# Performance work log

Measured on AMD Instinct MI355X. Metric: run time of the kernel, lower is better.

Reference implementation:

```python
import jax, jax.numpy as jnp
import numpy as np

B, T, C, H = 2, 2048, 1024, 16
D = C // H  # head dim = 64


def setup_inputs() -> dict:
    key = jax.random.key(0)
    ks = jax.random.split(key, 5)
    s = 0.02
    return {
        "x": jax.random.normal(ks[0], (B, T, C), dtype=jnp.float32),
        "c_attn_w": jax.random.normal(ks[1], (C, 3 * C), dtype=jnp.float32) * s,
        "c_attn_b": jax.random.normal(ks[2], (3 * C,), dtype=jnp.float32) * s,
        "c_proj_w": jax.random.normal(ks[3], (C, C), dtype=jnp.float32) * s,
        "c_proj_b": jax.random.normal(ks[4], (C,), dtype=jnp.float32) * s,
    }


def reference(x, c_attn_w, c_attn_b, c_proj_w, c_proj_b):
    b, t, c = x.shape
    # GPT-2 Conv1D: x @ W + b
    qkv = x @ c_attn_w + c_attn_b                      # [B,T,3C]
    q, k, v = jnp.split(qkv, 3, axis=-1)
    # [B,H,T,D]
    q = q.reshape(b, t, H, D).transpose(0, 2, 1, 3)
    k = k.reshape(b, t, H, D).transpose(0, 2, 1, 3)
    v = v.reshape(b, t, H, D).transpose(0, 2, 1, 3)
    scale = 1.0 / jnp.sqrt(jnp.float32(D))
    scores = jnp.einsum("bhqd,bhkd->bhqk", q, k) * scale  # [B,H,T,T]
    causal = jnp.tril(jnp.ones((t, t), dtype=bool))
    scores = jnp.where(causal, scores, jnp.float32(-jnp.inf))
    attn = jax.nn.softmax(scores, axis=-1)
    # drop_rate = 0.0 -> dropout is identity
    y = jnp.einsum("bhqk,bhkd->bhqd", attn, v)          # [B,H,T,D]
    y = y.transpose(0, 2, 1, 3).reshape(b, t, c)
    return y @ c_proj_w + c_proj_b
```

## Files before the change

kernel.cpp:

```cpp
#include <hip/hip_runtime.h>

#define B_ 2
#define T_ 2048
#define C_ 1024
#define H_ 16
#define D_ 64
#define M_ (B_ * T_)
#define NQKV_ (3 * C_)

typedef unsigned short us16;
typedef short bf16x8 __attribute__((ext_vector_type(8)));
typedef float f32x4 __attribute__((ext_vector_type(4)));

__device__ __forceinline__ f32x4 mfma16(bf16x8 a, bf16x8 b, f32x4 c) {
    return __builtin_amdgcn_mfma_f32_16x16x32_bf16(a, b, c, 0, 0, 0);
}

__device__ __forceinline__ us16 f2bf(float f) {
    union { float f; unsigned int u; } v; v.f = f;
    unsigned int r = v.u + 0x7fffu + ((v.u >> 16) & 1u);
    return (us16)(r >> 16);
}

__device__ __forceinline__ void gl_lds16(const us16* g, us16* l) {
    __builtin_amdgcn_global_load_lds(
        (const __attribute__((address_space(1))) void*)g,
        (__attribute__((address_space(3))) void*)l,
        16, 0, 0);
}

__global__ __launch_bounds__(256) void cvt_bf16(
    const float* __restrict__ in, us16* __restrict__ out, int n8)
{
    const int i = blockIdx.x * blockDim.x + threadIdx.x;
    if (i >= n8) return;
    const float4 a = ((const float4*)in)[2 * i];
    const float4 b = ((const float4*)in)[2 * i + 1];
    ushort4 lo = { f2bf(a.x), f2bf(a.y), f2bf(a.z), f2bf(a.w) };
    ushort4 hi = { f2bf(b.x), f2bf(b.y), f2bf(b.z), f2bf(b.w) };
    ((ushort4*)out)[2 * i] = lo;
    ((ushort4*)out)[2 * i + 1] = hi;
}

__global__ __launch_bounds__(256) void transpose_cvt(
    const float* __restrict__ W, us16* __restrict__ Wt, int K, int N)
{
    __shared__ float tile[32][33];
    const int n0 = blockIdx.x * 32, k0 = blockIdx.y * 32;
    const int t = threadIdx.x;
    {
        const int k = t >> 3, n4 = (t & 7) * 4;
        const float4 v = *(const float4*)(W + (size_t)(k0 + k) * N + n0 + n4);
        tile[k][n4 + 0] = v.x; tile[k][n4 + 1] = v.y;
        tile[k][n4 + 2] = v.z; tile[k][n4 + 3] = v.w;
    }
    __syncthreads();
    {
        const int n = t >> 3, k4 = (t & 7) * 4;
        ushort4 o = { f2bf(tile[k4 + 0][n]), f2bf(tile[k4 + 1][n]),
                      f2bf(tile[k4 + 2][n]), f2bf(tile[k4 + 3][n]) };
        *(ushort4*)(Wt + (size_t)(n0 + n) * K + k0 + k4) = o;
    }
}

__global__ __launch_bounds__(256) void gemm_bf16(
    const us16* __restrict__ A, const us16* __restrict__ Bt,
    const float* __restrict__ bias, void* __restrict__ Cout,
    int M, int N, int K, int out_bf16)
{
    __shared__ __align__(16) us16 smem[128 * 136];
    us16* sA = smem;
    us16* sB = smem + 128 * 64;

    const int tid = threadIdx.x;
    const int lane = tid & 63, wave = tid >> 6;
    const int wr = wave >> 1, wc = wave & 1;
    const int cq = lane & 15, quad = lane >> 4;
    const int m0 = blockIdx.y * 128, n0 = blockIdx.x * 128;

    const int srow  = lane >> 3;
    const int sgran = (lane & 7) ^ srow;
    const int scol  = sgran * 8;

    f32x4 acc[4][4];
    #pragma unroll
    for (int i = 0; i < 4; ++i)
        #pragma unroll
        for (int j = 0; j < 4; ++j)
            acc[i][j] = (f32x4){0.f, 0.f, 0.f, 0.f};

    for (int k0 = 0; k0 < K; k0 += 64) {
        #pragma unroll
        for (int p = 0; p < 4; ++p) {
            const int r = p * 32 + wave * 8;
            gl_lds16(A  + (size_t)(m0 + r + srow) * K + k0 + scol, sA + r * 64);
            gl_lds16(Bt + (size_t)(n0 + r + srow) * K + k0 + scol, sB + r * 64);
        }
        __syncthreads();

        #pragma unroll
        for (int kk = 0; kk < 64; kk += 32) {
            const int koS = (((kk >> 3) + quad) ^ (cq & 7)) << 3;
            bf16x8 af[4], bfg[4];
            #pragma unroll
            for (int i = 0; i < 4; ++i) {
                af[i]  = *(const bf16x8*)(sA + (wr * 64 + i * 16 + cq) * 64 + koS);
                bfg[i] = *(const bf16x8*)(sB + (wc * 64 + i * 16 + cq) * 64 + koS);
            }
            #pragma unroll
            for (int mi = 0; mi < 4; ++mi)
                #pragma unroll
                for (int ni = 0; ni < 4; ++ni)
                    acc[mi][ni] = mfma16(af[mi], bfg[ni], acc[mi][ni]);
        }
        __syncthreads();
    }

    if (out_bf16) {
        us16* Cs = smem;
        #pragma unroll
        for (int mi = 0; mi < 4; ++mi)
            #pragma unroll
            for (int ni = 0; ni < 4; ++ni) {
                const int n = n0 + wc * 64 + ni * 16 + cq;
                const float bv = bias[n];
                #pragma unroll
                for (int r = 0; r < 4; ++r)
                    Cs[(wr * 64 + mi * 16 + quad * 4 + r) * 136 +
                       wc * 64 + ni * 16 + cq] = f2bf(acc[mi][ni][r] + bv);
            }
        __syncthreads();
        us16* Co = (us16*)Cout;
        #pragma unroll
        for (int p = 0; p < 8; ++p) {
            const int chunk = p * 256 + tid;
            const int r = chunk >> 4, c = (chunk & 15) * 8;
            *(uint4*)(Co + (size_t)(m0 + r) * N + n0 + c) =
                *(const uint4*)(Cs + r * 136 + c);
        }
    } else {
        float* Co = (float*)Cout;
        #pragma unroll
        for (int mi = 0; mi < 4; ++mi)
            #pragma unroll
            for (int ni = 0; ni < 4; ++ni) {
                const int n = n0 + wc * 64 + ni * 16 + cq;
                const float bv = bias[n];
                #pragma unroll
                for (int r = 0; r < 4; ++r)
                    Co[(size_t)(m0 + wr * 64 + mi * 16 + quad * 4 + r) * N + n] =
                        acc[mi][ni][r] + bv;
            }
    }
}

__global__ __launch_bounds__(256) void attn_mfma(
    const us16* __restrict__ qkv, us16* __restrict__ y)
{
    __shared__ __align__(16) us16 Ks[64][72];
    __shared__ __align__(16) us16 Vt[64][72];
    __shared__ __align__(16) us16 Ps[64][72];

    const int tid = threadIdx.x;
    const int lane = tid & 63, wave = tid >> 6;
    const int cq = lane & 15, quad = lane >> 4;
    const int bh = blockIdx.x;
    const int qt = (int)gridDim.y - 1 - (int)blockIdx.y;
    const int b = bh >> 4, h = bh & 15;

    const us16* base = qkv + (size_t)b * T_ * NQKV_ + h * D_;

    bf16x8 qf[2];
    {
        const us16* qrow = base + (size_t)(qt * 64 + wave * 16 + cq) * NQKV_;
        qf[0] = *(const bf16x8*)(qrow + quad * 8);
        qf[1] = *(const bf16x8*)(qrow + 32 + quad * 8);
    }

    f32x4 ot[4];
    #pragma unroll
    for (int j = 0; j < 4; ++j) ot[j] = (f32x4){0.f, 0.f, 0.f, 0.f};
    f32x4 os = (f32x4){0.f, 0.f, 0.f, 0.f};

    const bf16x8 onesf = (bf16x8){16256, 16256, 16256, 16256,
                                  16256, 16256, 16256, 16256};

    const float ESCL = 0.125f;
    const float ESH  = -3.0f;

    const int kr0 = tid >> 3;
    const int kr1 = (256 + tid) >> 3;
    const int kc8 = (tid & 7) * 8;
    const int t2 = tid & 31, dc = tid >> 5;

    const us16* Kg = base + C_;
    const us16* Vg = base + 2 * C_;

    uint4 ka0 = *(const uint4*)(Kg + (size_t)kr0 * NQKV_ + kc8);
    uint4 ka1 = *(const uint4*)(Kg + (size_t)kr1 * NQKV_ + kc8);
    uint4 va0, va1;
    {
        const us16* vp = Vg + (size_t)(2 * t2) * NQKV_ + dc * 8;
        va0 = *(const uint4*)vp;
        va1 = *(const uint4*)(vp + NQKV_);
    }

    for (int kt = 0; kt <= qt; ++kt) {
        *(uint4*)(&Ks[kr0][kc8]) = ka0;
        *(uint4*)(&Ks[kr1][kc8]) = ka1;
        {
            const us16* p0 = (const us16*)&va0;
            const us16* p1 = (const us16*)&va1;
            #pragma unroll
            for (int j = 0; j < 8; ++j) {
                const unsigned int packed =
                    (unsigned int)p0[j] | ((unsigned int)p1[j] << 16);
                *(unsigned int*)(&Vt[dc * 8 + j][2 * t2]) = packed;
            }
        }
        __syncthreads();

        if (kt < qt) {
            const size_t ro = (size_t)((kt + 1) * 64);
            ka0 = *(const uint4*)(Kg + (ro + kr0) * NQKV_ + kc8);
            ka1 = *(const uint4*)(Kg + (ro + kr1) * NQKV_ + kc8);
            const us16* vp = Vg + (ro + 2 * t2) * NQKV_ + dc * 8;
            va0 = *(const uint4*)vp;
            va1 = *(const uint4*)(vp + NQKV_);
        }

        f32x4 s[4];
        #pragma unroll
        for (int j = 0; j < 4; ++j) {
            const bf16x8 kf0 = *(const bf16x8*)(&Ks[j * 16 + cq][quad * 8]);
            const bf16x8 kf1 = *(const bf16x8*)(&Ks[j * 16 + cq][32 + quad * 8]);
            f32x4 t = (f32x4){0.f, 0.f, 0.f, 0.f};
            t = mfma16(qf[0], kf0, t);
            t = mfma16(qf[1], kf1, t);
            s[j] = t;
        }

        float p[4][4];
        if (kt == qt) {
            const int qloc = wave * 16 + quad * 4;
            #pragma unroll
            for (int j = 0; j < 4; ++j) {
                const int kloc = j * 16 + cq;
                #pragma unroll
                for (int r = 0; r < 4; ++r) {
                    const float e = __expf(fmaf(s[j][r], ESCL, ESH));
                    p[j][r] = (kloc > qloc + r) ? 0.f : e;
                }
            }
        } else {
            #pragma unroll
            for (int j = 0; j < 4; ++j)
                #pragma unroll
                for (int r = 0; r < 4; ++r)
                    p[j][r] = __expf(fmaf(s[j][r], ESCL, ESH));
        }

        #pragma unroll
        for (int j = 0; j < 4; ++j)
            #pragma unroll
            for (int r = 0; r < 4; ++r) {
                union { float f; unsigned int u; } cv; cv.f = p[j][r];
                Ps[wave * 16 + quad * 4 + r][j * 16 + cq] =
                    (us16)(cv.u >> 16);
            }

        const bf16x8 pf0 = *(const bf16x8*)(&Ps[wave * 16 + cq][quad * 8]);
        const bf16x8 pf1 = *(const bf16x8*)(&Ps[wave * 16 + cq][32 + quad * 8]);

        os = mfma16(onesf, pf0, os);
        os = mfma16(onesf, pf1, os);
        #pragma unroll
        for (int dt = 0; dt < 4; ++dt) {
            const bf16x8 vf0 = *(const bf16x8*)(&Vt[dt * 16 + cq][quad * 8]);
            const bf16x8 vf1 = *(const bf16x8*)(&Vt[dt * 16 + cq][32 + quad * 8]);
            ot[dt] = mfma16(vf0, pf0, ot[dt]);
            ot[dt] = mfma16(vf1, pf1, ot[dt]);
        }

        __syncthreads();
    }

    const float inv = 1.0f / os[0];
    const int row = qt * 64 + wave * 16 + cq;
    us16* yp = y + (size_t)(b * T_ + row) * C_ + h * D_ + quad * 4;
    #pragma unroll
    for (int dt = 0; dt < 4; ++dt) {
        ushort4 ov = { f2bf(ot[dt][0] * inv), f2bf(ot[dt][1] * inv),
                       f2bf(ot[dt][2] * inv), f2bf(ot[dt][3] * inv) };
        *(ushort4*)(yp + dt * 16) = ov;
    }
}

extern "C" void kernel_launch(void* const* d_in, const int* in_sizes, int n_in,
                              void* d_out, int out_size, void* d_ws, size_t ws_size,
                              hipStream_t stream)
{
    const float* x  = (const float*)d_in[0];
    const float* aw = (const float*)d_in[1];
    const float* ab = (const float*)d_in[2];
    const float* pw = (const float*)d_in[3];
    const float* pb = (const float*)d_in[4];
    float* out = (float*)d_out;

    us16* xb   = (us16*)d_ws;
    us16* awT  = xb  + (size_t)M_ * C_;
    us16* pwT  = awT + (size_t)NQKV_ * C_;
    us16* qkvb = pwT + (size_t)C_ * C_;
    us16* yb   = qkvb + (size_t)M_ * NQKV_;

    cvt_bf16<<<(M_ * C_ / 8 + 255) / 256, 256, 0, stream>>>(x, xb, M_ * C_ / 8);
    transpose_cvt<<<dim3(NQKV_ / 32, C_ / 32), 256, 0, stream>>>(aw, awT, C_, NQKV_);
    transpose_cvt<<<dim3(C_ / 32, C_ / 32), 256, 0, stream>>>(pw, pwT, C_, C_);

    gemm_bf16<<<dim3(NQKV_ / 128, M_ / 128), 256, 0, stream>>>(
        xb, awT, ab, qkvb, M_, NQKV_, C_, 1);

    attn_mfma<<<dim3(B_ * H_, T_ / 64), 256, 0, stream>>>(qkvb, yb);

    gemm_bf16<<<dim3(C_ / 128, M_ / 128), 256, 0, stream>>>(
        yb, pwT, pb, out, M_, C_, C_, 0);
}
```

Baseline: 198.5 us.

## Split longest causal query tiles across two blocks with a combine kernel

```diff
diff --git a/kernel.cpp b/kernel.cpp
--- a/kernel.cpp
+++ b/kernel.cpp
@@ -155,7 +155,8 @@
 }
 
 __global__ __launch_bounds__(256) void attn_mfma(
-    const us16* __restrict__ qkv, us16* __restrict__ y)
+    const us16* __restrict__ qkv, us16* __restrict__ y,
+    float* __restrict__ Pp, float* __restrict__ lp)
 {
     __shared__ __align__(16) us16 Ks[64][72];
     __shared__ __align__(16) us16 Vt[64][72];
@@ -165,8 +166,16 @@
     const int lane = tid & 63, wave = tid >> 6;
     const int cq = lane & 15, quad = lane >> 4;
     const int bh = blockIdx.x;
-    const int qt = (int)gridDim.y - 1 - (int)blockIdx.y;
+    const int j = blockIdx.y;
     const int b = bh >> 4, h = bh & 15;
+
+    int qt, k0t, k1t, slot;
+    if (j < 4)       { qt = 19 - j;        k0t = 0;  k1t = qt; slot = -1; }
+    else if (j < 16) { qt = 31 - (j - 4);  const int lo = (qt + 2) >> 1;
+                       k0t = 0;  k1t = lo - 1; slot = (31 - qt) * 2; }
+    else if (j < 28) { qt = 31 - (j - 16); const int lo = (qt + 2) >> 1;
+                       k0t = lo; k1t = qt; slot = (31 - qt) * 2 + 1; }
+    else             { qt = 43 - j;        k0t = 0;  k1t = qt; slot = -1; }
 
     const us16* base = qkv + (size_t)b * T_ * NQKV_ + h * D_;
 
@@ -179,7 +188,7 @@
 
     f32x4 ot[4];
     #pragma unroll
-    for (int j = 0; j < 4; ++j) ot[j] = (f32x4){0.f, 0.f, 0.f, 0.f};
+    for (int jj = 0; jj < 4; ++jj) ot[jj] = (f32x4){0.f, 0.f, 0.f, 0.f};
     f32x4 os = (f32x4){0.f, 0.f, 0.f, 0.f};
 
     const bf16x8 onesf = (bf16x8){16256, 16256, 16256, 16256,
@@ -196,31 +205,31 @@
     const us16* Kg = base + C_;
     const us16* Vg = base + 2 * C_;
 
-    uint4 ka0 = *(const uint4*)(Kg + (size_t)kr0 * NQKV_ + kc8);
-    uint4 ka1 = *(const uint4*)(Kg + (size_t)kr1 * NQKV_ + kc8);
+    uint4 ka0 = *(const uint4*)(Kg + ((size_t)k0t * 64 + kr0) * NQKV_ + kc8);
+    uint4 ka1 = *(const uint4*)(Kg + ((size_t)k0t * 64 + kr1) * NQKV_ + kc8);
     uint4 va0, va1;
     {
-        const us16* vp = Vg + (size_t)(2 * t2) * NQKV_ + dc * 8;
+        const us16* vp = Vg + ((size_t)k0t * 64 + 2 * t2) * NQKV_ + dc * 8;
         va0 = *(const uint4*)vp;
         va1 = *(const uint4*)(vp + NQKV_);
     }
 
-    for (int kt = 0; kt <= qt; ++kt) {
+    for (int kt = k0t; kt <= k1t; ++kt) {
         *(uint4*)(&Ks[kr0][kc8]) = ka0;
         *(uint4*)(&Ks[kr1][kc8]) = ka1;
         {
             const us16* p0 = (const us16*)&va0;
             const us16* p1 = (const us16*)&va1;
             #pragma unroll
-            for (int j = 0; j < 8; ++j) {
+            for (int jj = 0; jj < 8; ++jj) {
                 const unsigned int packed =
-                    (unsigned int)p0[j] | ((unsigned int)p1[j] << 16);
-                *(unsigned int*)(&Vt[dc * 8 + j][2 * t2]) = packed;
-            }
-        }
-        __syncthreads();
-
-        if (kt < qt) {
+                    (unsigned int)p0[jj] | ((unsigned int)p1[jj] << 16);
+                *(unsigned int*)(&Vt[dc * 8 + jj][2 * t2]) = packed;
+            }
+        }
+        __syncthreads();
+
+        if (kt < k1t) {
             const size_t ro = (size_t)((kt + 1) * 64);
             ka0 = *(const uint4*)(Kg + (ro + kr0) * NQKV_ + kc8);
             ka1 = *(const uint4*)(Kg + (ro + kr1) * NQKV_ + kc8);
@@ -231,41 +240,41 @@
 
         f32x4 s[4];
         #pragma unroll
-        for (int j = 0; j < 4; ++j) {
-            const bf16x8 kf0 = *(const bf16x8*)(&Ks[j * 16 + cq][quad * 8]);
-            const bf16x8 kf1 = *(const bf16x8*)(&Ks[j * 16 + cq][32 + quad * 8]);
+        for (int jj = 0; jj < 4; ++jj) {
+            const bf16x8 kf0 = *(const bf16x8*)(&Ks[jj * 16 + cq][quad * 8]);
+            const bf16x8 kf1 = *(const bf16x8*)(&Ks[jj * 16 + cq][32 + quad * 8]);
             f32x4 t = (f32x4){0.f, 0.f, 0.f, 0.f};
             t = mfma16(qf[0], kf0, t);
             t = mfma16(qf[1], kf1, t);
-            s[j] = t;
+            s[jj] = t;
         }
 
         float p[4][4];
         if (kt == qt) {
             const int qloc = wave * 16 + quad * 4;
             #pragma unroll
-            for (int j = 0; j < 4; ++j) {
-                const int kloc = j * 16 + cq;
+            for (int jj = 0; jj < 4; ++jj) {
+                const int kloc = jj * 16 + cq;
                 #pragma unroll
                 for (int r = 0; r < 4; ++r) {
-                    const float e = __expf(fmaf(s[j][r], ESCL, ESH));
-                    p[j][r] = (kloc > qloc + r) ? 0.f : e;
+                    const float e = __expf(fmaf(s[jj][r], ESCL, ESH));
+                    p[jj][r] = (kloc > qloc + r) ? 0.f : e;
                 }
             }
         } else {
             #pragma unroll
-            for (int j = 0; j < 4; ++j)
+            for (int jj = 0; jj < 4; ++jj)
                 #pragma unroll
                 for (int r = 0; r < 4; ++r)
-                    p[j][r] = __expf(fmaf(s[j][r], ESCL, ESH));
-        }
-
-        #pragma unroll
-        for (int j = 0; j < 4; ++j)
+                    p[jj][r] = __expf(fmaf(s[jj][r], ESCL, ESH));
+        }
+
+        #pragma unroll
+        for (int jj = 0; jj < 4; ++jj)
             #pragma unroll
             for (int r = 0; r < 4; ++r) {
-                union { float f; unsigned int u; } cv; cv.f = p[j][r];
-                Ps[wave * 16 + quad * 4 + r][j * 16 + cq] =
+                union { float f; unsigned int u; } cv; cv.f = p[jj][r];
+                Ps[wave * 16 + quad * 4 + r][jj * 16 + cq] =
                     (us16)(cv.u >> 16);
             }
 
@@ -285,15 +294,54 @@
         __syncthreads();
     }
 
-    const float inv = 1.0f / os[0];
-    const int row = qt * 64 + wave * 16 + cq;
-    us16* yp = y + (size_t)(b * T_ + row) * C_ + h * D_ + quad * 4;
+    if (slot >= 0) {
+        const int sg = bh * 24 + slot;
+        float* Pb = Pp + (size_t)sg * 4096;
+        #pragma unroll
+        for (int dt = 0; dt < 4; ++dt)
+            #pragma unroll
+            for (int i = 0; i < 4; ++i)
+                Pb[(dt * 16 + quad * 4 + i) * 64 + wave * 16 + cq] = ot[dt][i];
+        if (quad == 0) lp[(size_t)sg * 64 + wave * 16 + cq] = os[0];
+    } else {
+        const float inv = 1.0f / os[0];
+        const int row = qt * 64 + wave * 16 + cq;
+        us16* yp = y + (size_t)(b * T_ + row) * C_ + h * D_ + quad * 4;
+        #pragma unroll
+        for (int dt = 0; dt < 4; ++dt) {
+            ushort4 ov = { f2bf(ot[dt][0] * inv), f2bf(ot[dt][1] * inv),
+                           f2bf(ot[dt][2] * inv), f2bf(ot[dt][3] * inv) };
+            *(ushort4*)(yp + dt * 16) = ov;
+        }
+    }
+}
+
+__global__ __launch_bounds__(256) void attn_combine(
+    const float* __restrict__ Pp, const float* __restrict__ lp,
+    us16* __restrict__ y)
+{
+    const int bh = blockIdx.x, si = blockIdx.y;
+    const int qt = 31 - si;
+    const int b = bh >> 4, h = bh & 15;
+    const int t = threadIdx.x;
+    const int q = t & 63, dg = t >> 6;
+
+    const size_t sgA = (size_t)bh * 24 + si * 2;
+    const float la = lp[sgA * 64 + q];
+    const float lb = lp[(sgA + 1) * 64 + q];
+    const float inv = 1.0f / (la + lb);
+    const float* PA = Pp + sgA * 4096;
+    const float* PB = PA + 4096;
+
+    __align__(16) us16 ob[16];
     #pragma unroll
-    for (int dt = 0; dt < 4; ++dt) {
-        ushort4 ov = { f2bf(ot[dt][0] * inv), f2bf(ot[dt][1] * inv),
-                       f2bf(ot[dt][2] * inv), f2bf(ot[dt][3] * inv) };
-        *(ushort4*)(yp + dt * 16) = ov;
-    }
+    for (int i = 0; i < 16; ++i) {
+        const int d = dg * 16 + i;
+        ob[i] = f2bf((PA[d * 64 + q] + PB[d * 64 + q]) * inv);
+    }
+    us16* yp = y + (size_t)(b * T_ + qt * 64 + q) * C_ + h * D_ + dg * 16;
+    *(uint4*)(yp)     = *(const uint4*)(&ob[0]);
+    *(uint4*)(yp + 8) = *(const uint4*)(&ob[8]);
 }
 
 extern "C" void kernel_launch(void* const* d_in, const int* in_sizes, int n_in,
@@ -313,6 +361,9 @@
     us16* qkvb = pwT + (size_t)C_ * C_;
     us16* yb   = qkvb + (size_t)M_ * NQKV_;
 
+    float* Pp = (float*)d_ws;
+    float* lp = Pp + (size_t)768 * 4096;
+
     cvt_bf16<<<(M_ * C_ / 8 + 255) / 256, 256, 0, stream>>>(x, xb, M_ * C_ / 8);
     transpose_cvt<<<dim3(NQKV_ / 32, C_ / 32), 256, 0, stream>>>(aw, awT, C_, NQKV_);
     transpose_cvt<<<dim3(C_ / 32, C_ / 32), 256, 0, stream>>>(pw, pwT, C_, C_);
@@ -320,7 +371,8 @@
     gemm_bf16<<<dim3(NQKV_ / 128, M_ / 128), 256, 0, stream>>>(
         xb, awT, ab, qkvb, M_, NQKV_, C_, 1);
 
-    attn_mfma<<<dim3(B_ * H_, T_ / 64), 256, 0, stream>>>(qkvb, yb);
+    attn_mfma<<<dim3(B_ * H_, 44), 256, 0, stream>>>(qkvb, yb, Pp, lp);
+    attn_combine<<<dim3(B_ * H_, 12), 256, 0, stream>>>(Pp, lp, yb);
 
     gemm_bf16<<<dim3(C_ / 128, M_ / 128), 256, 0, stream>>>(
         yb, pwT, pb, out, M_, C_, C_, 0);
```

New measurement: 198.1 us. Within noise of the previous version (-0.2%).
